# Performance work log

Hardware: AMD Instinct MI355X
Metric: run time of the kernel (lower is better)

Reference implementation:

```python
import jax, jax.numpy as jnp
import numpy as np

UNITS = 512
INPUT_DIM = 64
BATCH = 131072


def setup_inputs() -> dict:
    key = jax.random.key(0)
    kx, kw = jax.random.split(key)
    x = jax.random.normal(kx, (BATCH, INPUT_DIM), dtype=jnp.float32)
    w = jax.random.normal(kw, (UNITS, INPUT_DIM), dtype=jnp.float32) * 0.05
    return {"x": x, "w": w}


def reference(x, w):
    # Pairwise squared L2 distance: dist[b, u] = sum_d (w[u,d] - x[b,d])^2
    # avoids the O(B*U*D) broadcast intermediate).
    x_sq = jnp.sum(x * x, axis=-1, keepdims=True)        # [B, 1]
    w_sq = jnp.sum(w * w, axis=-1)[None, :]              # [1, U]
    cross = jnp.einsum("bd,ud->bu", x, w)                # [B, U]
    return x_sq + w_sq - 2.0 * cross
```

## Files before the change

### kernel.cpp

```cpp
#include <hip/hip_runtime.h>

#define BATCH 131072
#define UNITS 512
#define DIM   64
#define BM    128

typedef __attribute__((ext_vector_type(8))) short  short8;
typedef __attribute__((ext_vector_type(4))) float  floatx4;

static __device__ __forceinline__ unsigned short f32_to_bf16(float f) {
    union { float f; unsigned int u; } c; c.f = f;
    unsigned int u = c.u;
    unsigned int r = u + 0x7fffu + ((u >> 16) & 1u);
    return (unsigned short)(r >> 16);
}

__global__ __launch_bounds__(256) void prep_w_kernel(
    const float* __restrict__ w,
    unsigned short* __restrict__ wb,
    float* __restrict__ wsq)
{
    const int u = blockIdx.x * 4 + (threadIdx.x >> 6);
    const int d = threadIdx.x & 63;
    float v = w[u * DIM + d];
    wb[u * DIM + d] = f32_to_bf16(v);
    float s = v * v;
    #pragma unroll
    for (int o = 32; o > 0; o >>= 1) s += __shfl_xor(s, o);
    if (d == 0) wsq[u] = s;
}

__global__ __launch_bounds__(256) void dist_kernel(
    const float* __restrict__ x,
    const unsigned short* __restrict__ wb,
    const float* __restrict__ wsq,
    float* __restrict__ out)
{
    __shared__ __align__(16) unsigned short xb[BM][DIM];
    __shared__ float xsq[BM];

    const int tid  = threadIdx.x;
    const int row0 = blockIdx.x * BM;

    #pragma unroll
    for (int half = 0; half < BM / 64; ++half) {
        const int r = half * 64 + (tid >> 2);
        const int q = tid & 3;
        const float4* src = (const float4*)(x + (size_t)(row0 + r) * DIM + q * 16);
        float v[16];
        *(float4*)&v[0]  = src[0];
        *(float4*)&v[4]  = src[1];
        *(float4*)&v[8]  = src[2];
        *(float4*)&v[12] = src[3];
        float s = 0.f;
        unsigned short p[16];
        #pragma unroll
        for (int i = 0; i < 16; ++i) { s += v[i] * v[i]; p[i] = f32_to_bf16(v[i]); }
        uint4* dst = (uint4*)&xb[r][q * 16];
        dst[0] = *(uint4*)&p[0];
        dst[1] = *(uint4*)&p[8];
        s += __shfl_xor(s, 1);
        s += __shfl_xor(s, 2);
        if (q == 0) xsq[r] = s;
    }
    __syncthreads();

    const int wave = tid >> 6;
    const int lane = tid & 63;
    const int l15  = lane & 15;
    const int quad = lane >> 4;
    const int mrow = wave * 32;

    const short8* arow0 = (const short8*)&xb[mrow + l15][0];
    const short8* arow1 = (const short8*)&xb[mrow + 16 + l15][0];
    const short8 a00 = arow0[quad];
    const short8 a01 = arow0[quad + 4];
    const short8 a10 = arow1[quad];
    const short8 a11 = arow1[quad + 4];

    float xs0[4], xs1[4];
    #pragma unroll
    for (int i = 0; i < 4; ++i) {
        xs0[i] = xsq[mrow + quad * 4 + i];
        xs1[i] = xsq[mrow + 16 + quad * 4 + i];
    }

    const short8* wv = (const short8*)wb;

    for (int ut = 0; ut < UNITS / 16; ++ut) {
        const int ubase = ut * 16;
        const short8 b0 = wv[(ubase + l15) * 8 + quad];
        const short8 b1 = wv[(ubase + l15) * 8 + quad + 4];
        floatx4 acc0 = {0.f, 0.f, 0.f, 0.f};
        floatx4 acc1 = {0.f, 0.f, 0.f, 0.f};
        acc0 = __builtin_amdgcn_mfma_f32_16x16x32_bf16(a00, b0, acc0, 0, 0, 0);
        acc0 = __builtin_amdgcn_mfma_f32_16x16x32_bf16(a01, b1, acc0, 0, 0, 0);
        acc1 = __builtin_amdgcn_mfma_f32_16x16x32_bf16(a10, b0, acc1, 0, 0, 0);
        acc1 = __builtin_amdgcn_mfma_f32_16x16x32_bf16(a11, b1, acc1, 0, 0, 0);

        const float wq = wsq[ubase + l15];
        const int col = ubase + l15;
        #pragma unroll
        for (int i = 0; i < 4; ++i) {
            const size_t r0i = (size_t)(row0 + mrow + quad * 4 + i) * UNITS + col;
            const size_t r1i = (size_t)(row0 + mrow + 16 + quad * 4 + i) * UNITS + col;
            __builtin_nontemporal_store(xs0[i] + wq - 2.0f * acc0[i], &out[r0i]);
            __builtin_nontemporal_store(xs1[i] + wq - 2.0f * acc1[i], &out[r1i]);
        }
    }
}

extern "C" void kernel_launch(void* const* d_in, const int* in_sizes, int n_in,
                              void* d_out, int out_size, void* d_ws, size_t ws_size,
                              hipStream_t stream) {
    const float* x = (const float*)d_in[0];
    const float* w = (const float*)d_in[1];
    float* out = (float*)d_out;

    unsigned short* wb  = (unsigned short*)d_ws;
    float*          wsq = (float*)((char*)d_ws + UNITS * DIM * 2);

    prep_w_kernel<<<UNITS / 4, 256, 0, stream>>>(w, wb, wsq);
    dist_kernel<<<BATCH / BM, 256, 0, stream>>>(x, wb, wsq, out);
}
```

Baseline: 318.9 us.

## Stage output tiles through padded LDS for 16-byte coalesced stores

Each wave now computes a 16x64 output tile (four MFMA column tiles at once) and writes the results into a padded per-wave LDS buffer. It then reads them back as float4 and issues 16-byte nontemporal stores covering contiguous 256-byte row segments, instead of scattered 4-byte stores. The w squared norms are also cached in shared memory, and the B fragments are loaded in groups of four. The goal is better write coalescing on this output-bandwidth-bound kernel, at the cost of extra LDS traffic, more shared memory and no barrier, which is valid because each wave only touches its own buffer.

New measurement: 293.8 us. 1.09x faster.

```diff
diff --git a/kernel.cpp b/kernel.cpp
--- a/kernel.cpp
+++ b/kernel.cpp
@@ -4,6 +4,7 @@
 #define UNITS 512
 #define DIM   64
 #define BM    128
+#define STRIDE 68
 
 typedef __attribute__((ext_vector_type(8))) short  short8;
 typedef __attribute__((ext_vector_type(4))) float  floatx4;
@@ -38,9 +39,14 @@
 {
     __shared__ __align__(16) unsigned short xb[BM][DIM];
     __shared__ float xsq[BM];
+    __shared__ float wsq_s[UNITS];
+    __shared__ __align__(16) float st[4][16][STRIDE];
 
     const int tid  = threadIdx.x;
     const int row0 = blockIdx.x * BM;
+
+    wsq_s[tid]       = wsq[tid];
+    wsq_s[tid + 256] = wsq[tid + 256];
 
     #pragma unroll
     for (int half = 0; half < BM / 64; ++half) {
@@ -71,41 +77,59 @@
     const int quad = lane >> 4;
     const int mrow = wave * 32;
 
-    const short8* arow0 = (const short8*)&xb[mrow + l15][0];
-    const short8* arow1 = (const short8*)&xb[mrow + 16 + l15][0];
-    const short8 a00 = arow0[quad];
-    const short8 a01 = arow0[quad + 4];
-    const short8 a10 = arow1[quad];
-    const short8 a11 = arow1[quad + 4];
-
-    float xs0[4], xs1[4];
+    short8 a[2][2];
+    float  xs[2][4];
     #pragma unroll
-    for (int i = 0; i < 4; ++i) {
-        xs0[i] = xsq[mrow + quad * 4 + i];
-        xs1[i] = xsq[mrow + 16 + quad * 4 + i];
+    for (int mf = 0; mf < 2; ++mf) {
+        const short8* ar = (const short8*)&xb[mrow + mf * 16 + l15][0];
+        a[mf][0] = ar[quad];
+        a[mf][1] = ar[quad + 4];
+        #pragma unroll
+        for (int i = 0; i < 4; ++i)
+            xs[mf][i] = xsq[mrow + mf * 16 + quad * 4 + i];
     }
 
-    const short8* wv = (const short8*)wb;
+    const short8* wv  = (const short8*)wb;
+    float*        stw = &st[wave][0][0];
 
-    for (int ut = 0; ut < UNITS / 16; ++ut) {
-        const int ubase = ut * 16;
-        const short8 b0 = wv[(ubase + l15) * 8 + quad];
-        const short8 b1 = wv[(ubase + l15) * 8 + quad + 4];
-        floatx4 acc0 = {0.f, 0.f, 0.f, 0.f};
-        floatx4 acc1 = {0.f, 0.f, 0.f, 0.f};
-        acc0 = __builtin_amdgcn_mfma_f32_16x16x32_bf16(a00, b0, acc0, 0, 0, 0);
-        acc0 = __builtin_amdgcn_mfma_f32_16x16x32_bf16(a01, b1, acc0, 0, 0, 0);
-        acc1 = __builtin_amdgcn_mfma_f32_16x16x32_bf16(a10, b0, acc1, 0, 0, 0);
-        acc1 = __builtin_amdgcn_mfma_f32_16x16x32_bf16(a11, b1, acc1, 0, 0, 0);
+    for (int gu = 0; gu < 8; ++gu) {
+        const int colb = gu * 64;
 
-        const float wq = wsq[ubase + l15];
-        const int col = ubase + l15;
+        short8 b[4][2];
+        float  wq[4];
         #pragma unroll
-        for (int i = 0; i < 4; ++i) {
-            const size_t r0i = (size_t)(row0 + mrow + quad * 4 + i) * UNITS + col;
-            const size_t r1i = (size_t)(row0 + mrow + 16 + quad * 4 + i) * UNITS + col;
-            __builtin_nontemporal_store(xs0[i] + wq - 2.0f * acc0[i], &out[r0i]);
-            __builtin_nontemporal_store(xs1[i] + wq - 2.0f * acc1[i], &out[r1i]);
+        for (int t = 0; t < 4; ++t) {
+            const short8* bp = wv + (size_t)(colb + t * 16 + l15) * 8;
+            b[t][0] = bp[quad];
+            b[t][1] = bp[quad + 4];
+            wq[t]   = wsq_s[colb + t * 16 + l15];
+        }
+
+        #pragma unroll
+        for (int mf = 0; mf < 2; ++mf) {
+            floatx4 acc[4];
+            #pragma unroll
+            for (int t = 0; t < 4; ++t) {
+                acc[t] = floatx4{0.f, 0.f, 0.f, 0.f};
+                acc[t] = __builtin_amdgcn_mfma_f32_16x16x32_bf16(a[mf][0], b[t][0], acc[t], 0, 0, 0);
+                acc[t] = __builtin_amdgcn_mfma_f32_16x16x32_bf16(a[mf][1], b[t][1], acc[t], 0, 0, 0);
+            }
+
+            #pragma unroll
+            for (int t = 0; t < 4; ++t)
+                #pragma unroll
+                for (int i = 0; i < 4; ++i)
+                    stw[(quad * 4 + i) * STRIDE + t * 16 + l15] =
+                        xs[mf][i] + wq[t] - 2.0f * acc[t][i];
+
+            #pragma unroll
+            for (int j = 0; j < 4; ++j) {
+                const int r = quad + 4 * j;
+                const floatx4 v = *(const floatx4*)&stw[r * STRIDE + l15 * 4];
+                float* dst = out + (size_t)(row0 + mrow + mf * 16 + r) * UNITS
+                                 + colb + l15 * 4;
+                __builtin_nontemporal_store(v, (floatx4*)dst);
+            }
         }
     }
 }
```
